# Kernel optimization log

Hardware: AMD Instinct MI355X
Metric: run time of the kernel (lower is better)

## Reference

```python
import jax, jax.numpy as jnp
import numpy as np
from jax import lax

B, E, H, L, P, IMG, NCLS = 8, 768, 12, 12, 16, 224, 1000
D = E // H
MLP = 4 * E
SCALE = D ** -0.5
NPATCH = (IMG // P) ** 2  # 196
N = NPATCH + 1             # 197 with cls token
INIT_VAL = 0.1


def _ln(x, g, b, eps=1e-5):
    mu = jnp.mean(x, -1, keepdims=True)
    var = jnp.mean((x - mu) ** 2, -1, keepdims=True)
    return (x - mu) / jnp.sqrt(var + eps) * g + b


def _wasserstein(q, cov_q, k, cov_k):
    # 2-Wasserstein distance matrix between diagonal Gaussians (STOSA style)
    mean_term = (-2.0 * jnp.einsum('bhnd,bhmd->bhnm', q, k)
                 + jnp.sum(q * q, -1)[..., :, None]
                 + jnp.sum(k * k, -1)[..., None, :])
    sq_q = jnp.sqrt(jnp.clip(cov_q, 1e-24))
    sq_k = jnp.sqrt(jnp.clip(cov_k, 1e-24))
    cov_term = (-2.0 * jnp.einsum('bhnd,bhmd->bhnm', sq_q, sq_k)
                + jnp.sum(cov_q, -1)[..., :, None]
                + jnp.sum(cov_k, -1)[..., None, :])
    return mean_term + cov_term


def _patch_embed(x, w, b):
    # x: [B,3,IMG,IMG], w: [E,3,P,P] -> [B, NPATCH, E]
    y = lax.conv_general_dilated(x, w, (P, P), 'VALID',
                                 dimension_numbers=('NCHW', 'OIHW', 'NCHW'))
    y = y + b[None, :, None, None]
    return y.reshape(x.shape[0], E, -1).transpose(0, 2, 1)


def _mlp(x, w1, b1, w2, b2):
    return jax.nn.gelu(x @ w1.T + b1, approximate=False) @ w2.T + b2


def setup_inputs() -> dict:
    key = jax.random.key(0)
    ks = jax.random.split(key, 32)
    s = 0.02
    inp = {
        'x': jax.random.normal(ks[0], (B, 3, IMG, IMG), jnp.float32),
        'rel_pos_bias': jax.random.normal(ks[1], (H, N, N), jnp.float32),
        'patch_w': jax.random.normal(ks[2], (E, 3, P, P), jnp.float32) * s,
        'patch_b': jnp.zeros((E,), jnp.float32),
        'cov_patch_w': jax.random.normal(ks[3], (E, 3, P, P), jnp.float32) * s,
        'cov_patch_b': jnp.zeros((E,), jnp.float32),
        'cls_tok': jax.random.normal(ks[4], (1, 1, E), jnp.float32) * s,
        'cov_cls_tok': jax.random.normal(ks[5], (1, 1, E), jnp.float32) * s,
        'norm1_g': jnp.ones((L, E), jnp.float32),
        'norm1_b': jnp.zeros((L, E), jnp.float32),
        'qkv_w': jax.random.normal(ks[6], (L, 3 * E, E), jnp.float32) * s,
        'q_bias': jnp.zeros((L, E), jnp.float32),
        'v_bias': jnp.zeros((L, E), jnp.float32),
        'cov_q_bias': jnp.zeros((L, E), jnp.float32),
        'cov_v_bias': jnp.zeros((L, E), jnp.float32),
        'proj_w': jax.random.normal(ks[7], (L, E, E), jnp.float32) * s,
        'proj_b': jnp.zeros((L, E), jnp.float32),
        'cov_proj_w': jax.random.normal(ks[8], (L, E, E), jnp.float32) * s,
        'cov_proj_b': jnp.zeros((L, E), jnp.float32),
        'gamma1': jnp.full((L, E), INIT_VAL, jnp.float32),
        'gamma2': jnp.full((L, E), INIT_VAL, jnp.float32),
        'norm2_g': jnp.ones((L, E), jnp.float32),
        'norm2_b': jnp.zeros((L, E), jnp.float32),
        'fc1_w': jax.random.normal(ks[9], (L, MLP, E), jnp.float32) * s,
        'fc1_b': jnp.zeros((L, MLP), jnp.float32),
        'fc2_w': jax.random.normal(ks[10], (L, E, MLP), jnp.float32) * s,
        'fc2_b': jnp.zeros((L, E), jnp.float32),
        'fc_norm_g': jnp.ones((E,), jnp.float32),
        'fc_norm_b': jnp.zeros((E,), jnp.float32),
        'head_w': jax.random.normal(ks[11], (NCLS, E), jnp.float32) * s,
        'head_b': jnp.zeros((NCLS,), jnp.float32),
    }
    # fix_init_weight rescaling: proj / cov_proj / fc2 divided by sqrt(2*layer_id)
    resc = 1.0 / jnp.sqrt(2.0 * jnp.arange(1, L + 1, dtype=jnp.float32))
    inp['proj_w'] = inp['proj_w'] * resc[:, None, None]
    inp['cov_proj_w'] = inp['cov_proj_w'] * resc[:, None, None]
    inp['fc2_w'] = inp['fc2_w'] * resc[:, None, None]
    return inp


def reference(x, rel_pos_bias, patch_w, patch_b, cov_patch_w, cov_patch_b,
              cls_tok, cov_cls_tok, norm1_g, norm1_b, qkv_w, q_bias, v_bias,
              cov_q_bias, cov_v_bias, proj_w, proj_b, cov_proj_w, cov_proj_b,
              gamma1, gamma2, norm2_g, norm2_b, fc1_w, fc1_b, fc2_w, fc2_b,
              fc_norm_g, fc_norm_b, head_w, head_b):
    b = x.shape[0]
    xm = _patch_embed(x, patch_w, patch_b)
    xc = _patch_embed(x, cov_patch_w, cov_patch_b)
    xm = jnp.concatenate([jnp.broadcast_to(cls_tok, (b, 1, E)), xm], 1)
    xc = jnp.concatenate([jnp.broadcast_to(cov_cls_tok, (b, 1, E)), xc], 1)
    n = xm.shape[1]

    for i in range(L):
        xm_n = _ln(xm, norm1_g[i], norm1_b[i])
        xc_n = _ln(xc, norm1_g[i], norm1_b[i])  # shared norm1, as in source
        qkvb = jnp.concatenate([q_bias[i], jnp.zeros_like(v_bias[i]), v_bias[i]])
        cov_qkvb = jnp.concatenate([cov_q_bias[i], jnp.zeros_like(cov_v_bias[i]), cov_v_bias[i]])
        qkv = (xm_n @ qkv_w[i].T + qkvb).reshape(b, n, 3, H, D).transpose(2, 0, 3, 1, 4)
        q, k, v = qkv[0], qkv[1], qkv[2]
        # NOTE: source (bug-faithfully) uses qkv.weight for the cov path too
        cqkv = jax.nn.elu(xc_n @ qkv_w[i].T + cov_qkvb) + 1.0
        cqkv = cqkv.reshape(b, n, 3, H, D).transpose(2, 0, 3, 1, 4)
        cq, ck, cv = cqkv[0], cqkv[1], cqkv[2]
        q = q * SCALE
        attn = jax.nn.sigmoid(-_wasserstein(q, cq, k, ck) + 1e-24)
        attn = jax.nn.softmax(attn + rel_pos_bias, axis=-1)  # [B,H,N,N]
        mean_ctx = jnp.einsum('bhnm,bhmd->bhnd', attn, v).transpose(0, 2, 1, 3).reshape(b, n, E)
        cov_ctx = jnp.einsum('bhnm,bhmd->bhnd', attn * attn, cv).transpose(0, 2, 1, 3).reshape(b, n, E)
        mh = mean_ctx @ proj_w[i].T + proj_b[i]
        ch = cov_ctx @ cov_proj_w[i].T + cov_proj_b[i]
        xm = xm + gamma1[i] * mh
        xm = xm + gamma2[i] * _mlp(_ln(xm, norm2_g[i], norm2_b[i]), fc1_w[i], fc1_b[i], fc2_w[i], fc2_b[i])
        xc = xc + gamma1[i] * ch
        xc = xc + gamma2[i] * _mlp(_ln(xc, norm2_g[i], norm2_b[i]), fc1_w[i], fc1_b[i], fc2_w[i], fc2_b[i])

    t = jnp.mean(xm[:, 1:], axis=1)          # mean pooling over patch tokens
    t = _ln(t, fc_norm_g, fc_norm_b)
    return t @ head_w.T + head_b              # [B, num_classes]
```

## Files before the change

kernel.cpp:

```cpp
#include <hip/hip_runtime.h>
#include <hip/hip_bf16.h>
#include <math.h>

#define BB 8
#define EE 768
#define HH 12
#define LL 12
#define DD 64
#define MLPD 3072
#define NN 197
#define NPATCH 196
#define NCLS 1000
#define NROWS (BB*NN)
#define PROWS (BB*NPATCH)
#define MPAD 1664
#define HTILES 13
#define NBH (BB*HH)
#define NP224 224
#define NP256 256
#define SCALE 0.125f

#define MODE_F32   0
#define MODE_ELU1F 1
#define MODE_GELUB 2
#define MODE_RESF  3

typedef __attribute__((ext_vector_type(8))) short bf16x8;
typedef __attribute__((ext_vector_type(4))) float f32x4;

__device__ __forceinline__ unsigned short f2b(float f) {
    union { __hip_bfloat16 h; unsigned short u; } x;
    x.h = __float2bfloat16(f);
    return x.u;
}

__device__ __forceinline__ float b2f(unsigned short u) {
    union { unsigned int i; float f; } x;
    x.i = ((unsigned int)u) << 16;
    return x.f;
}

#define GLD(gptr, lptr) __builtin_amdgcn_global_load_lds( \
    (const __attribute__((address_space(1))) unsigned int*)(gptr), \
    (__attribute__((address_space(3))) unsigned int*)(lptr), 16, 0, 0)

__global__ __launch_bounds__(256) void mfma_gemm2(
    const unsigned short* __restrict__ A0, const unsigned short* __restrict__ A1,
    const unsigned short* __restrict__ W0, const unsigned short* __restrict__ W1,
    const float* __restrict__ bias0, const float* __restrict__ bias1,
    int K, int Nc, int mode0, int mode1,
    const float* __restrict__ gamma,
    const float* __restrict__ resid0, const float* __restrict__ resid1,
    float* __restrict__ Cf0, float* __restrict__ Cf1,
    unsigned short* __restrict__ Cb0, unsigned short* __restrict__ Cb1)
{
    __shared__ unsigned short lA[128 * 32];
    __shared__ unsigned short lB[128 * 32];
    const int tid  = threadIdx.x;
    const int lane = tid & 63;
    const int wave = tid >> 6;
    const int wm = wave >> 1, wn = wave & 1;
    const int half = blockIdx.y >= HTILES;
    const int mout0 = (blockIdx.y - (half ? HTILES : 0)) * 128;
    const int n0 = blockIdx.x * 128;
    const unsigned short* A = half ? A1 : A0;
    const unsigned short* W = half ? W1 : W0;
    const float* bias = half ? bias1 : bias0;
    const float* resid = half ? resid1 : resid0;
    float* Cf = half ? Cf1 : Cf0;
    unsigned short* Cb = half ? Cb1 : Cb0;
    const int mode = half ? mode1 : mode0;

    const int srow  = lane >> 2;
    const int skoff = (lane & 3) * 8;
    const int fr = lane & 15;
    const int fk = (lane >> 4) * 8;

    f32x4 acc[4][4];
#pragma unroll
    for (int i = 0; i < 4; i++)
#pragma unroll
        for (int j = 0; j < 4; j++) acc[i][j] = (f32x4){0.f, 0.f, 0.f, 0.f};

    for (int k0 = 0; k0 < K; k0 += 32) {
#pragma unroll
        for (int i = 0; i < 2; i++) {
            int chunk = wave * 2 + i;
            int row = chunk * 16 + srow;
            GLD(A + (size_t)(mout0 + row) * K + k0 + skoff, lA + chunk * 512);
            GLD(W + (size_t)(n0 + row) * K + k0 + skoff, lB + chunk * 512);
        }
        __syncthreads();
        bf16x8 a[4], b[4];
#pragma unroll
        for (int t = 0; t < 4; t++) {
            a[t] = *(const bf16x8*)(lA + (wm * 64 + t * 16 + fr) * 32 + fk);
            b[t] = *(const bf16x8*)(lB + (wn * 64 + t * 16 + fr) * 32 + fk);
        }
#pragma unroll
        for (int i = 0; i < 4; i++)
#pragma unroll
            for (int j = 0; j < 4; j++)
                acc[i][j] = __builtin_amdgcn_mfma_f32_16x16x32_bf16(a[i], b[j], acc[i][j], 0, 0, 0);
        __syncthreads();
    }

    const int crow0 = mout0 + wm * 64;
    const int ccol0 = n0 + wn * 64;
    const int lr = (lane >> 4) * 4;
    const int lc = lane & 15;
#pragma unroll
    for (int i = 0; i < 4; i++) {
#pragma unroll
        for (int j = 0; j < 4; j++) {
            int col = ccol0 + j * 16 + lc;
            float bv = bias ? bias[col] : 0.f;
#pragma unroll
            for (int r = 0; r < 4; r++) {
                int row = crow0 + i * 16 + lr + r;
                float v = acc[i][j][r] + bv;
                size_t o = (size_t)row * Nc + col;
                if (mode == MODE_ELU1F) {
                    Cf[o] = (v > 0.f) ? (v + 1.f) : expf(v);
                } else if (mode == MODE_GELUB) {
                    v = 0.5f * v * (1.f + erff(v * 0.70710678118654752f));
                    Cb[o] = f2b(v);
                } else if (mode == MODE_RESF) {
                    Cf[o] = resid[o] + gamma[col] * v;
                } else {
                    Cf[o] = v;
                }
            }
        }
    }
}

__global__ __launch_bounds__(256) void mfma_gemm2_sk(
    const unsigned short* __restrict__ A0, const unsigned short* __restrict__ A1,
    const unsigned short* __restrict__ W0, const unsigned short* __restrict__ W1,
    int K, int Kc, int Nc, int S,
    float* __restrict__ P)
{
    __shared__ unsigned short lA[128 * 32];
    __shared__ unsigned short lB[128 * 32];
    const int tid  = threadIdx.x;
    const int lane = tid & 63;
    const int wave = tid >> 6;
    const int wm = wave >> 1, wn = wave & 1;
    const int half = blockIdx.y >= HTILES;
    const int mout0 = (blockIdx.y - (half ? HTILES : 0)) * 128;
    const int n0 = blockIdx.x * 128;
    const int z = blockIdx.z;
    const int kb = z * Kc;
    const unsigned short* A = half ? A1 : A0;
    const unsigned short* W = half ? W1 : W0;

    const int srow  = lane >> 2;
    const int skoff = (lane & 3) * 8;
    const int fr = lane & 15;
    const int fk = (lane >> 4) * 8;

    f32x4 acc[4][4];
#pragma unroll
    for (int i = 0; i < 4; i++)
#pragma unroll
        for (int j = 0; j < 4; j++) acc[i][j] = (f32x4){0.f, 0.f, 0.f, 0.f};

    for (int k0 = kb; k0 < kb + Kc; k0 += 32) {
#pragma unroll
        for (int i = 0; i < 2; i++) {
            int chunk = wave * 2 + i;
            int row = chunk * 16 + srow;
            GLD(A + (size_t)(mout0 + row) * K + k0 + skoff, lA + chunk * 512);
            GLD(W + (size_t)(n0 + row) * K + k0 + skoff, lB + chunk * 512);
        }
        __syncthreads();
        bf16x8 a[4], b[4];
#pragma unroll
        for (int t = 0; t < 4; t++) {
            a[t] = *(const bf16x8*)(lA + (wm * 64 + t * 16 + fr) * 32 + fk);
            b[t] = *(const bf16x8*)(lB + (wn * 64 + t * 16 + fr) * 32 + fk);
        }
#pragma unroll
        for (int i = 0; i < 4; i++)
#pragma unroll
            for (int j = 0; j < 4; j++)
                acc[i][j] = __builtin_amdgcn_mfma_f32_16x16x32_bf16(a[i], b[j], acc[i][j], 0, 0, 0);
        __syncthreads();
    }

    float* Pout = P + (size_t)(half * S + z) * MPAD * Nc;
    const int crow0 = mout0 + wm * 64;
    const int ccol0 = n0 + wn * 64;
    const int lr = (lane >> 4) * 4;
    const int lc = lane & 15;
#pragma unroll
    for (int i = 0; i < 4; i++) {
#pragma unroll
        for (int j = 0; j < 4; j++) {
            int col = ccol0 + j * 16 + lc;
#pragma unroll
            for (int r = 0; r < 4; r++) {
                int row = crow0 + i * 16 + lr + r;
                Pout[(size_t)row * Nc + col] = acc[i][j][r];
            }
        }
    }
}

__global__ __launch_bounds__(256) void sk_reduce_kernel(
    const float* __restrict__ P, int S, int Nc, int mode,
    const float* __restrict__ bias0, const float* __restrict__ bias1,
    const float* __restrict__ gamma,
    const float* __restrict__ resid0, const float* __restrict__ resid1,
    float* __restrict__ C0, float* __restrict__ C1)
{
    const size_t per = (size_t)MPAD * Nc;
    size_t gi = ((size_t)blockIdx.x * 256 + threadIdx.x) * 4;
    if (gi >= per) return;
    const int half = blockIdx.y;
    const float* p = P + (size_t)half * S * per + gi;
    float4 s = *(const float4*)p;
    for (int z = 1; z < S; z++) {
        float4 q = *(const float4*)(p + (size_t)z * per);
        s.x += q.x; s.y += q.y; s.z += q.z; s.w += q.w;
    }
    const int col = (int)(gi % (size_t)Nc);
    const float* bias = half ? bias1 : bias0;
    float4 bv = *(const float4*)(bias + col);
    s.x += bv.x; s.y += bv.y; s.z += bv.z; s.w += bv.w;
    float* C = half ? C1 : C0;
    if (mode == MODE_RESF) {
        const float* resid = half ? resid1 : resid0;
        float4 rv = *(const float4*)(resid + gi);
        float4 gv = *(const float4*)(gamma + col);
        s.x = rv.x + gv.x * s.x;
        s.y = rv.y + gv.y * s.y;
        s.z = rv.z + gv.z * s.z;
        s.w = rv.w + gv.w * s.w;
    }
    *(float4*)(C + gi) = s;
}

__global__ __launch_bounds__(256) void pre_kernel(
    const float* __restrict__ qkv, const float* __restrict__ cqkv,
    unsigned short* __restrict__ Aq, unsigned short* __restrict__ Bk,
    float* __restrict__ rsum, float* __restrict__ csum,
    unsigned short* __restrict__ vT, unsigned short* __restrict__ cvT)
{
    const int t = blockIdx.x;
    const int bh = blockIdx.y;
    const int b = bh / HH, h = bh % HH;
    const int n0 = t * 64;
    const int lane = threadIdx.x & 63;
    const int w = threadIdx.x >> 6;
    __shared__ unsigned short vs[64][66];
    __shared__ unsigned short cvs[64][66];

    for (int p = 0; p < 16; p++) {
        int nl = p * 4 + w;
        int n = n0 + nl;
        int d = lane;
        size_t arow = ((size_t)bh * NP256 + n) * 128;
        if (n < NN) {
            size_t basei = (size_t)(b * NN + n) * 3 * EE + h * DD + d;
            float q  = qkv[basei];
            float k  = qkv[basei + EE];
            float v  = qkv[basei + 2 * EE];
            float cq = cqkv[basei];
            float ck = cqkv[basei + EE];
            float cv = cqkv[basei + 2 * EE];
            float qs = q * SCALE;
            float sqq = sqrtf(fmaxf(cq, 1e-24f));
            float sqk = sqrtf(fmaxf(ck, 1e-24f));
            Aq[arow + d]      = f2b(qs);
            Aq[arow + 64 + d] = f2b(sqq);
            Bk[arow + d]      = f2b(k);
            Bk[arow + 64 + d] = f2b(sqk);
            vs[nl][d]  = f2b(v);
            cvs[nl][d] = f2b(cv);
            float r = qs * qs + cq;
            float c = k * k + ck;
            for (int off2 = 32; off2 > 0; off2 >>= 1) {
                r += __shfl_down(r, off2);
                c += __shfl_down(c, off2);
            }
            if (d == 0) { rsum[bh * NP256 + n] = r; csum[bh * NP256 + n] = c; }
        } else {
            ((unsigned int*)(Aq + arow))[d] = 0u;
            ((unsigned int*)(Bk + arow))[d] = 0u;
            vs[nl][d] = 0; cvs[nl][d] = 0;
            if (d == 0) { rsum[bh * NP256 + n] = 0.f; csum[bh * NP256 + n] = 0.f; }
        }
    }
    __syncthreads();
    for (int p = 0; p < 16; p++) {
        int dr = p * 4 + w;
        int n = n0 + lane;
        if (n < NP224) {
            vT [((size_t)bh * 64 + dr) * NP224 + n] = vs[lane][dr];
            cvT[((size_t)bh * 64 + dr) * NP224 + n] = cvs[lane][dr];
        }
    }
}

#define PADW 232
__global__ __launch_bounds__(256) void attn_fused(
    const unsigned short* __restrict__ Aq, const unsigned short* __restrict__ Bk,
    const float* __restrict__ rsum, const float* __restrict__ csum,
    const float* __restrict__ rpb,
    const unsigned short* __restrict__ vT, const unsigned short* __restrict__ cvT,
    unsigned short* __restrict__ ctxm, unsigned short* __restrict__ ctxc)
{
    __shared__ unsigned short lA[64 * 32];
    __shared__ unsigned short lB[256 * 32];
    __shared__ unsigned short lB2[128 * 32];
    __shared__ unsigned short pL[64 * PADW];
    const int tid = threadIdx.x, lane = tid & 63, w = tid >> 6;
    const int bh = blockIdx.y;
    const int b = bh / HH, h = bh % HH;
    const int q0 = blockIdx.x * 64;
    const int srow = lane >> 2, skoff = (lane & 3) * 8;
    const int fr = lane & 15, fk = (lane >> 4) * 8;
    const int lr4 = (lane >> 4) * 4;
    const unsigned short* A = Aq + (size_t)bh * NP256 * 128;
    const unsigned short* B = Bk + (size_t)bh * NP256 * 128;

    f32x4 accS[16];
#pragma unroll
    for (int j = 0; j < 16; j++) accS[j] = (f32x4){0.f, 0.f, 0.f, 0.f};

    for (int k0 = 0; k0 < 128; k0 += 32) {
        GLD(A + (size_t)(q0 + w * 16 + srow) * 128 + k0 + skoff, lA + w * 512);
#pragma unroll
        for (int i = 0; i < 4; i++) {
            int chunk = w * 4 + i;
            GLD(B + (size_t)(chunk * 16 + srow) * 128 + k0 + skoff, lB + chunk * 512);
        }
        __syncthreads();
        bf16x8 a = *(const bf16x8*)(lA + (w * 16 + fr) * 32 + fk);
#pragma unroll
        for (int j = 0; j < 16; j++) {
            bf16x8 bb = *(const bf16x8*)(lB + (j * 16 + fr) * 32 + fk);
            accS[j] = __builtin_amdgcn_mfma_f32_16x16x32_bf16(a, bb, accS[j], 0, 0, 0);
        }
        __syncthreads();
    }

    float rs[4];
#pragma unroll
    for (int r = 0; r < 4; r++) rs[r] = rsum[bh * NP256 + q0 + w * 16 + lr4 + r];
    float cs[16];
#pragma unroll
    for (int j = 0; j < 16; j++) cs[j] = csum[bh * NP256 + j * 16 + fr];

#pragma unroll
    for (int r = 0; r < 4; r++) {
        int rowg = q0 + w * 16 + lr4 + r;
        float v[16];
#pragma unroll
        for (int j = 0; j < 16; j++) {
            int col = j * 16 + fr;
            float z = 2.f * accS[j][r] - rs[r] - cs[j] + 1e-24f;
            float s = 1.f / (1.f + expf(-z));
            float rp = (col < NN && rowg < NN) ? rpb[((size_t)h * NN + rowg) * NN + col] : 0.f;
            v[j] = (col < NN) ? (s + rp) : -1e30f;
        }
        float mx = -1e30f;
#pragma unroll
        for (int j = 0; j < 16; j++) mx = fmaxf(mx, v[j]);
        mx = fmaxf(mx, __shfl_xor(mx, 1));
        mx = fmaxf(mx, __shfl_xor(mx, 2));
        mx = fmaxf(mx, __shfl_xor(mx, 4));
        mx = fmaxf(mx, __shfl_xor(mx, 8));
        float sum = 0.f;
#pragma unroll
        for (int j = 0; j < 16; j++) { v[j] = expf(v[j] - mx); sum += v[j]; }
        sum += __shfl_xor(sum, 1);
        sum += __shfl_xor(sum, 2);
        sum += __shfl_xor(sum, 4);
        sum += __shfl_xor(sum, 8);
        float inv = 1.f / sum;
        int rowl = w * 16 + lr4 + r;
#pragma unroll
        for (int j = 0; j < 14; j++)
            pL[rowl * PADW + j * 16 + fr] = f2b(v[j] * inv);
    }

    f32x4 acc2[2][4];
#pragma unroll
    for (int p = 0; p < 2; p++)
#pragma unroll
        for (int j = 0; j < 4; j++) acc2[p][j] = (f32x4){0.f, 0.f, 0.f, 0.f};

    for (int k0 = 0; k0 < NP224; k0 += 32) {
#pragma unroll
        for (int i = 0; i < 2; i++) {
            int chunk = w * 2 + i;
            const unsigned short* src = (chunk < 4)
                ? (vT  + ((size_t)bh * 64 + chunk * 16 + srow) * NP224)
                : (cvT + ((size_t)bh * 64 + (chunk - 4) * 16 + srow) * NP224);
            GLD(src + k0 + skoff, lB2 + chunk * 512);
        }
        __syncthreads();
        bf16x8 ap = *(const bf16x8*)(pL + (w * 16 + fr) * PADW + k0 + fk);
        bf16x8 ap2;
#pragma unroll
        for (int e = 0; e < 8; e++) {
            float pv = b2f((unsigned short)ap[e]);
            ap2[e] = (short)f2b(pv * pv);
        }
#pragma unroll
        for (int j = 0; j < 4; j++) {
            bf16x8 bv = *(const bf16x8*)(lB2 + (j * 16 + fr) * 32 + fk);
            bf16x8 bc = *(const bf16x8*)(lB2 + ((64 + j * 16) + fr) * 32 + fk);
            acc2[0][j] = __builtin_amdgcn_mfma_f32_16x16x32_bf16(ap,  bv, acc2[0][j], 0, 0, 0);
            acc2[1][j] = __builtin_amdgcn_mfma_f32_16x16x32_bf16(ap2, bc, acc2[1][j], 0, 0, 0);
        }
        __syncthreads();
    }

#pragma unroll
    for (int j = 0; j < 4; j++) {
        int d = j * 16 + fr;
#pragma unroll
        for (int r = 0; r < 4; r++) {
            int n = q0 + w * 16 + lr4 + r;
            if (n >= NN) continue;
            size_t o = ((size_t)(b * NN + n)) * EE + h * DD + d;
            ctxm[o] = f2b(acc2[0][j][r]);
            ctxc[o] = f2b(acc2[1][j][r]);
        }
    }
}

__global__ __launch_bounds__(256) void head_kernel(
    const float* __restrict__ pooled, const float* __restrict__ W,
    const float* __restrict__ bias, float* __restrict__ out)
{
    const int wv = threadIdx.x >> 6, lane = threadIdx.x & 63;
    const int c = blockIdx.x * 4 + wv;
    const int b = blockIdx.y;
    if (c >= NCLS) return;
    const float* wr = W + (size_t)c * EE;
    const float* pr = pooled + (size_t)b * EE;
    float s = 0.f;
#pragma unroll
    for (int i = 0; i < 12; i++) s += pr[lane + i * 64] * wr[lane + i * 64];
    for (int off = 32; off > 0; off >>= 1) s += __shfl_down(s, off);
    if (lane == 0) out[(size_t)b * NCLS + c] = s + bias[c];
}

__global__ __launch_bounds__(256) void cvt_kernel(
    const float* __restrict__ src, unsigned short* __restrict__ dst, int n)
{
    int i = (blockIdx.x * 256 + threadIdx.x) * 4;
    if (i >= n) return;
    float4 f = *(const float4*)(src + i);
    ushort4 u;
    u.x = f2b(f.x); u.y = f2b(f.y); u.z = f2b(f.z); u.w = f2b(f.w);
    *(ushort4*)(dst + i) = u;
}

#define W_QKV   0
#define W_PROJ  1769472
#define W_CPROJ 2359296
#define W_FC1   2949120
#define W_FC2   5308416
#define W_TOTAL 7667712

__global__ __launch_bounds__(256) void cvt_layer_kernel(
    const float* __restrict__ qkvw, const float* __restrict__ pw,
    const float* __restrict__ cpw, const float* __restrict__ f1,
    const float* __restrict__ f2, unsigned short* __restrict__ dst)
{
    int i = (blockIdx.x * 256 + threadIdx.x) * 4;
    if (i >= W_TOTAL) return;
    const float* s; int off;
    if (i < W_PROJ)        { s = qkvw; off = W_QKV; }
    else if (i < W_CPROJ)  { s = pw;   off = W_PROJ; }
    else if (i < W_FC1)    { s = cpw;  off = W_CPROJ; }
    else if (i < W_FC2)    { s = f1;   off = W_FC1; }
    else                   { s = f2;   off = W_FC2; }
    float4 f = *(const float4*)(s + (i - off));
    ushort4 u;
    u.x = f2b(f.x); u.y = f2b(f.y); u.z = f2b(f.z); u.w = f2b(f.w);
    *(ushort4*)(dst + i) = u;
}

__global__ __launch_bounds__(256) void im2col_kernel(
    const float* __restrict__ x, unsigned short* __restrict__ col)
{
    int idx = blockIdx.x * 256 + threadIdx.x;
    if (idx >= PROWS * EE) return;
    int c = idx % EE;
    int r = idx / EE;
    int b = r / NPATCH;
    int p = r % NPATCH;
    int ph = p / 14, pw = p % 14;
    int ch = c >> 8;
    int rem = c & 255;
    int i = rem >> 4, j = rem & 15;
    col[idx] = f2b(x[(((size_t)b * 3 + ch) * 224 + (ph * 16 + i)) * 224 + (pw * 16 + j)]);
}

__global__ __launch_bounds__(256) void assemble_kernel(
    const float* __restrict__ tm, const float* __restrict__ tc,
    const float* __restrict__ cls, const float* __restrict__ ccls,
    float* __restrict__ xm, float* __restrict__ xc)
{
    int idx = blockIdx.x * 256 + threadIdx.x;
    if (idx >= NROWS * EE) return;
    int e = idx % EE;
    int r = idx / EE;
    int b = r / NN, n = r % NN;
    if (n == 0) {
        xm[idx] = cls[e];
        xc[idx] = ccls[e];
    } else {
        size_t s = ((size_t)(b * NPATCH + n - 1)) * EE + e;
        xm[idx] = tm[s];
        xc[idx] = tc[s];
    }
}

__global__ __launch_bounds__(256) void ln2_kernel(
    const float* __restrict__ xm, const float* __restrict__ xc,
    unsigned short* __restrict__ y, const float* __restrict__ g,
    const float* __restrict__ bb)
{
    int row = blockIdx.x;
    int tid = threadIdx.x;
    const float* src;
    size_t orow;
    if (row < NROWS) { src = xm + (size_t)row * EE; orow = row; }
    else { src = xc + (size_t)(row - NROWS) * EE; orow = (size_t)(row - NROWS) + MPAD; }
    __shared__ float red[256];
    float v0 = src[tid], v1 = src[tid + 256], v2 = src[tid + 512];
    red[tid] = v0 + v1 + v2;
    __syncthreads();
    for (int s = 128; s > 0; s >>= 1) { if (tid < s) red[tid] += red[tid + s]; __syncthreads(); }
    float mu = red[0] * (1.f / 768.f);
    __syncthreads();
    float d0 = v0 - mu, d1 = v1 - mu, d2 = v2 - mu;
    red[tid] = d0 * d0 + d1 * d1 + d2 * d2;
    __syncthreads();
    for (int s = 128; s > 0; s >>= 1) { if (tid < s) red[tid] += red[tid + s]; __syncthreads(); }
    float rstd = rsqrtf(red[0] * (1.f / 768.f) + 1e-5f);
    unsigned short* yr = y + orow * EE;
    yr[tid]       = f2b(d0 * rstd * g[tid]       + bb[tid]);
    yr[tid + 256] = f2b(d1 * rstd * g[tid + 256] + bb[tid + 256]);
    yr[tid + 512] = f2b(d2 * rstd * g[tid + 512] + bb[tid + 512]);
}

__global__ __launch_bounds__(256) void qkvbias_kernel(
    const float* __restrict__ qb, const float* __restrict__ vb,
    const float* __restrict__ cqb, const float* __restrict__ cvb,
    float* __restrict__ bm, float* __restrict__ bc)
{
    int j = blockIdx.x * 256 + threadIdx.x;
    if (j >= 3 * EE) return;
    float m, c;
    if (j < EE)        { m = qb[j];        c = cqb[j]; }
    else if (j < 2*EE) { m = 0.f;          c = 0.f; }
    else               { m = vb[j - 2*EE]; c = cvb[j - 2*EE]; }
    bm[j] = m;
    bc[j] = c;
}

__global__ __launch_bounds__(256) void pool_ln_kernel(
    const float* __restrict__ xm, float* __restrict__ out,
    const float* __restrict__ g, const float* __restrict__ bb)
{
    int b = blockIdx.x;
    int tid = threadIdx.x;
    __shared__ float red[256];
    float p[3];
#pragma unroll
    for (int i = 0; i < 3; i++) {
        int e = tid + i * 256;
        float s = 0.f;
        for (int n = 1; n < NN; n++) s += xm[((size_t)(b * NN + n)) * EE + e];
        p[i] = s * (1.f / 196.f);
    }
    red[tid] = p[0] + p[1] + p[2];
    __syncthreads();
    for (int s = 128; s > 0; s >>= 1) { if (tid < s) red[tid] += red[tid + s]; __syncthreads(); }
    float mu = red[0] * (1.f / 768.f);
    __syncthreads();
    float d0 = p[0] - mu, d1 = p[1] - mu, d2 = p[2] - mu;
    red[tid] = d0 * d0 + d1 * d1 + d2 * d2;
    __syncthreads();
    for (int s = 128; s > 0; s >>= 1) { if (tid < s) red[tid] += red[tid + s]; __syncthreads(); }
    float rstd = rsqrtf(red[0] * (1.f / 768.f) + 1e-5f);
    out[(size_t)b * EE + tid]       = d0 * rstd * g[tid]       + bb[tid];
    out[(size_t)b * EE + tid + 256] = d1 * rstd * g[tid + 256] + bb[tid + 256];
    out[(size_t)b * EE + tid + 512] = d2 * rstd * g[tid + 512] + bb[tid + 512];
}

extern "C" void kernel_launch(void* const* d_in, const int* in_sizes, int n_in,
                              void* d_out, int out_size, void* d_ws, size_t ws_size,
                              hipStream_t stream)
{
    const float* x        = (const float*)d_in[0];
    const float* rpb      = (const float*)d_in[1];
    const float* patch_w  = (const float*)d_in[2];
    const float* patch_b  = (const float*)d_in[3];
    const float* cpatch_w = (const float*)d_in[4];
    const float* cpatch_b = (const float*)d_in[5];
    const float* cls_tok  = (const float*)d_in[6];
    const float* ccls_tok = (const float*)d_in[7];
    const float* norm1_g  = (const float*)d_in[8];
    const float* norm1_b  = (const float*)d_in[9];
    const float* qkv_w    = (const float*)d_in[10];
    const float* q_bias   = (const float*)d_in[11];
    const float* v_bias   = (const float*)d_in[12];
    const float* cq_bias  = (const float*)d_in[13];
    const float* cv_bias  = (const float*)d_in[14];
    const float* proj_w   = (const float*)d_in[15];
    const float* proj_b   = (const float*)d_in[16];
    const float* cproj_w  = (const float*)d_in[17];
    const float* cproj_b  = (const float*)d_in[18];
    const float* gamma1   = (const float*)d_in[19];
    const float* gamma2   = (const float*)d_in[20];
    const float* norm2_g  = (const float*)d_in[21];
    const float* norm2_b  = (const float*)d_in[22];
    const float* fc1_w    = (const float*)d_in[23];
    const float* fc1_b    = (const float*)d_in[24];
    const float* fc2_w    = (const float*)d_in[25];
    const float* fc2_b    = (const float*)d_in[26];
    const float* fcn_g    = (const float*)d_in[27];
    const float* fcn_b    = (const float*)d_in[28];
    const float* head_w   = (const float*)d_in[29];
    const float* head_b   = (const float*)d_in[30];
    float* out = (float*)d_out;

    char* base = (char*)d_ws;
    size_t off = 0;
    auto alloc = [&](size_t bytes) {
        void* p = base + off;
        off = (off + bytes + 255) & ~(size_t)255;
        return p;
    };
    unsigned short* wbuf  = (unsigned short*)alloc((size_t)W_TOTAL * 2);
    unsigned short* pw_m  = (unsigned short*)alloc((size_t)589824 * 2);
    unsigned short* pw_c  = (unsigned short*)alloc((size_t)589824 * 2);
    float* xm   = (float*)alloc((size_t)MPAD * EE * 4);
    float* xc   = (float*)alloc((size_t)MPAD * EE * 4);
    unsigned short* xn2 = (unsigned short*)alloc((size_t)2 * MPAD * EE * 2);
    float* qkv  = (float*)alloc((size_t)MPAD * 3 * EE * 4);
    float* cqkv = (float*)alloc((size_t)MPAD * 3 * EE * 4);
    unsigned short* hbuf = (unsigned short*)alloc((size_t)2 * MPAD * MLPD * 2);
    unsigned short* Aq  = (unsigned short*)alloc((size_t)NBH * NP256 * 128 * 2);
    unsigned short* Bk  = (unsigned short*)alloc((size_t)NBH * NP256 * 128 * 2);
    unsigned short* vT  = (unsigned short*)alloc((size_t)NBH * 64 * NP224 * 2);
    unsigned short* cvT = (unsigned short*)alloc((size_t)NBH * 64 * NP224 * 2);
    float* rsum = (float*)alloc((size_t)NBH * NP256 * 4);
    float* csum = (float*)alloc((size_t)NBH * NP256 * 4);
    unsigned short* ctx2 = (unsigned short*)alloc((size_t)2 * MPAD * EE * 2);
    unsigned short* colb = (unsigned short*)alloc((size_t)MPAD * EE * 2);
    float* biasq  = (float*)alloc(3 * EE * 4);
    float* biasc  = (float*)alloc(3 * EE * 4);
    float* pooled = (float*)alloc((size_t)BB * EE * 4);
    float* pbuf = (float*)alloc((size_t)2 * 4 * MPAD * EE * 4);
    float* tm = qkv;
    float* tc = cqkv;
    unsigned short* ctxm = ctx2;
    unsigned short* ctxc = ctx2 + (size_t)MPAD * EE;

    dim3 t256(256);
    dim3 gridRed(MPAD * EE / 1024, 2);

    cvt_kernel<<<dim3(589824 / 4 / 256), t256, 0, stream>>>(patch_w, pw_m, 589824);
    cvt_kernel<<<dim3(589824 / 4 / 256), t256, 0, stream>>>(cpatch_w, pw_c, 589824);
    im2col_kernel<<<dim3((PROWS * EE + 255) / 256), t256, 0, stream>>>(x, colb);
    mfma_gemm2_sk<<<dim3(EE / 128, 2 * HTILES, 3), t256, 0, stream>>>(
        colb, colb, pw_m, pw_c, EE, 256, EE, 3, pbuf);
    sk_reduce_kernel<<<gridRed, t256, 0, stream>>>(
        pbuf, 3, EE, MODE_F32, patch_b, cpatch_b, nullptr, nullptr, nullptr, tm, tc);
    assemble_kernel<<<dim3((NROWS * EE + 255) / 256), t256, 0, stream>>>(
        tm, tc, cls_tok, ccls_tok, xm, xc);

    dim3 gridQKV(3 * EE / 128, 2 * HTILES);
    dim3 gridMLP(MLPD / 128, 2 * HTILES);
    dim3 gridPre(4, NBH);
    dim3 gridAttn(4, NBH);
    dim3 gridCvtL((W_TOTAL / 4 + 255) / 256);
    dim3 gridLN(2 * NROWS);
    const unsigned short* xn2c = xn2 + (size_t)MPAD * EE;
    const unsigned short* hbufc = hbuf + (size_t)MPAD * MLPD;

    for (int l = 0; l < LL; l++) {
        cvt_layer_kernel<<<gridCvtL, t256, 0, stream>>>(
            qkv_w + (size_t)l * 3 * EE * EE, proj_w + (size_t)l * EE * EE,
            cproj_w + (size_t)l * EE * EE, fc1_w + (size_t)l * MLPD * EE,
            fc2_w + (size_t)l * EE * MLPD, wbuf);
        qkvbias_kernel<<<dim3(9), t256, 0, stream>>>(
            q_bias + l * EE, v_bias + l * EE, cq_bias + l * EE, cv_bias + l * EE,
            biasq, biasc);

        ln2_kernel<<<gridLN, t256, 0, stream>>>(xm, xc, xn2, norm1_g + l * EE, norm1_b + l * EE);
        mfma_gemm2<<<gridQKV, t256, 0, stream>>>(
            xn2, xn2c, wbuf + W_QKV, wbuf + W_QKV, biasq, biasc, EE, 3 * EE,
            MODE_F32, MODE_ELU1F, nullptr, nullptr, nullptr, qkv, cqkv, nullptr, nullptr);

        pre_kernel<<<gridPre, t256, 0, stream>>>(qkv, cqkv, Aq, Bk, rsum, csum, vT, cvT);
        attn_fused<<<gridAttn, t256, 0, stream>>>(Aq, Bk, rsum, csum, rpb, vT, cvT, ctxm, ctxc);

        mfma_gemm2_sk<<<dim3(EE / 128, 2 * HTILES, 3), t256, 0, stream>>>(
            ctxm, ctxc, wbuf + W_PROJ, wbuf + W_CPROJ, EE, 256, EE, 3, pbuf);
        sk_reduce_kernel<<<gridRed, t256, 0, stream>>>(
            pbuf, 3, EE, MODE_RESF, proj_b + l * EE, cproj_b + l * EE,
            gamma1 + l * EE, xm, xc, xm, xc);

        ln2_kernel<<<gridLN, t256, 0, stream>>>(xm, xc, xn2, norm2_g + l * EE, norm2_b + l * EE);
        mfma_gemm2<<<gridMLP, t256, 0, stream>>>(
            xn2, xn2c, wbuf + W_FC1, wbuf + W_FC1, fc1_b + l * MLPD, fc1_b + l * MLPD,
            EE, MLPD, MODE_GELUB, MODE_GELUB, nullptr, nullptr, nullptr,
            nullptr, nullptr, hbuf, hbuf + (size_t)MPAD * MLPD);
        mfma_gemm2_sk<<<dim3(EE / 128, 2 * HTILES, 4), t256, 0, stream>>>(
            hbuf, hbufc, wbuf + W_FC2, wbuf + W_FC2, MLPD, 768, EE, 4, pbuf);
        sk_reduce_kernel<<<gridRed, t256, 0, stream>>>(
            pbuf, 4, EE, MODE_RESF, fc2_b + l * EE, fc2_b + l * EE,
            gamma2 + l * EE, xm, xc, xm, xc);
    }

    pool_ln_kernel<<<dim3(BB), t256, 0, stream>>>(xm, pooled, fcn_g, fcn_b);
    head_kernel<<<dim3((NCLS + 3) / 4, BB), t256, 0, stream>>>(pooled, head_w, head_b, out);
}
```

Before: 2.880 ms.

## Double-buffer GEMM LDS, fuse split-K reduce with LayerNorm, hoist weight conversion

Three unrelated changes. The GEMM kernels now double-buffer their LDS tiles so the next K-slice loads while MFMAs run on the current one. The split-K reduce is fused with the residual update and the following LayerNorm, which removes the separate ln2 launches inside the layer loop. Weight and bias conversion for all 12 layers now happens once before the loop instead of per layer, at the cost of a larger bf16 weight buffer and doubled LDS per block, which may reduce occupancy.

```diff
diff --git a/kernel.cpp b/kernel.cpp
--- a/kernel.cpp
+++ b/kernel.cpp
@@ -54,8 +54,8 @@
     float* __restrict__ Cf0, float* __restrict__ Cf1,
     unsigned short* __restrict__ Cb0, unsigned short* __restrict__ Cb1)
 {
-    __shared__ unsigned short lA[128 * 32];
-    __shared__ unsigned short lB[128 * 32];
+    __shared__ unsigned short lA[2][128 * 32];
+    __shared__ unsigned short lB[2][128 * 32];
     const int tid  = threadIdx.x;
     const int lane = tid & 63;
     const int wave = tid >> 6;
@@ -76,26 +76,33 @@
     const int fr = lane & 15;
     const int fk = (lane >> 4) * 8;
 
-    f32x4 acc[4][4];
-#pragma unroll
-    for (int i = 0; i < 4; i++)
-#pragma unroll
-        for (int j = 0; j < 4; j++) acc[i][j] = (f32x4){0.f, 0.f, 0.f, 0.f};
-
-    for (int k0 = 0; k0 < K; k0 += 32) {
+    auto stage = [&](int bufi, int k0) {
 #pragma unroll
         for (int i = 0; i < 2; i++) {
             int chunk = wave * 2 + i;
             int row = chunk * 16 + srow;
-            GLD(A + (size_t)(mout0 + row) * K + k0 + skoff, lA + chunk * 512);
-            GLD(W + (size_t)(n0 + row) * K + k0 + skoff, lB + chunk * 512);
-        }
-        __syncthreads();
+            GLD(A + (size_t)(mout0 + row) * K + k0 + skoff, &lA[bufi][chunk * 512]);
+            GLD(W + (size_t)(n0 + row) * K + k0 + skoff, &lB[bufi][chunk * 512]);
+        }
+    };
+
+    f32x4 acc[4][4];
+#pragma unroll
+    for (int i = 0; i < 4; i++)
+#pragma unroll
+        for (int j = 0; j < 4; j++) acc[i][j] = (f32x4){0.f, 0.f, 0.f, 0.f};
+
+    const int NT = K >> 5;
+    stage(0, 0);
+    __syncthreads();
+    int cur = 0;
+    for (int t = 0; t < NT; t++) {
+        if (t + 1 < NT) stage(cur ^ 1, (t + 1) * 32);
         bf16x8 a[4], b[4];
 #pragma unroll
-        for (int t = 0; t < 4; t++) {
-            a[t] = *(const bf16x8*)(lA + (wm * 64 + t * 16 + fr) * 32 + fk);
-            b[t] = *(const bf16x8*)(lB + (wn * 64 + t * 16 + fr) * 32 + fk);
+        for (int q = 0; q < 4; q++) {
+            a[q] = *(const bf16x8*)(&lA[cur][(wm * 64 + q * 16 + fr) * 32 + fk]);
+            b[q] = *(const bf16x8*)(&lB[cur][(wn * 64 + q * 16 + fr) * 32 + fk]);
         }
 #pragma unroll
         for (int i = 0; i < 4; i++)
@@ -103,6 +110,7 @@
             for (int j = 0; j < 4; j++)
                 acc[i][j] = __builtin_amdgcn_mfma_f32_16x16x32_bf16(a[i], b[j], acc[i][j], 0, 0, 0);
         __syncthreads();
+        cur ^= 1;
     }
 
     const int crow0 = mout0 + wm * 64;
@@ -141,8 +149,8 @@
     int K, int Kc, int Nc, int S,
     float* __restrict__ P)
 {
-    __shared__ unsigned short lA[128 * 32];
-    __shared__ unsigned short lB[128 * 32];
+    __shared__ unsigned short lA[2][128 * 32];
+    __shared__ unsigned short lB[2][128 * 32];
     const int tid  = threadIdx.x;
     const int lane = tid & 63;
     const int wave = tid >> 6;
@@ -160,26 +168,33 @@
     const int fr = lane & 15;
     const int fk = (lane >> 4) * 8;
 
-    f32x4 acc[4][4];
-#pragma unroll
-    for (int i = 0; i < 4; i++)
-#pragma unroll
-        for (int j = 0; j < 4; j++) acc[i][j] = (f32x4){0.f, 0.f, 0.f, 0.f};
-
-    for (int k0 = kb; k0 < kb + Kc; k0 += 32) {
+    auto stage = [&](int bufi, int k0) {
 #pragma unroll
         for (int i = 0; i < 2; i++) {
             int chunk = wave * 2 + i;
             int row = chunk * 16 + srow;
-            GLD(A + (size_t)(mout0 + row) * K + k0 + skoff, lA + chunk * 512);
-            GLD(W + (size_t)(n0 + row) * K + k0 + skoff, lB + chunk * 512);
-        }
-        __syncthreads();
+            GLD(A + (size_t)(mout0 + row) * K + k0 + skoff, &lA[bufi][chunk * 512]);
+            GLD(W + (size_t)(n0 + row) * K + k0 + skoff, &lB[bufi][chunk * 512]);
+        }
+    };
+
+    f32x4 acc[4][4];
+#pragma unroll
+    for (int i = 0; i < 4; i++)
+#pragma unroll
+        for (int j = 0; j < 4; j++) acc[i][j] = (f32x4){0.f, 0.f, 0.f, 0.f};
+
+    const int NT = Kc >> 5;
+    stage(0, kb);
+    __syncthreads();
+    int cur = 0;
+    for (int t = 0; t < NT; t++) {
+        if (t + 1 < NT) stage(cur ^ 1, kb + (t + 1) * 32);
         bf16x8 a[4], b[4];
 #pragma unroll
-        for (int t = 0; t < 4; t++) {
-            a[t] = *(const bf16x8*)(lA + (wm * 64 + t * 16 + fr) * 32 + fk);
-            b[t] = *(const bf16x8*)(lB + (wn * 64 + t * 16 + fr) * 32 + fk);
+        for (int q = 0; q < 4; q++) {
+            a[q] = *(const bf16x8*)(&lA[cur][(wm * 64 + q * 16 + fr) * 32 + fk]);
+            b[q] = *(const bf16x8*)(&lB[cur][(wn * 64 + q * 16 + fr) * 32 + fk]);
         }
 #pragma unroll
         for (int i = 0; i < 4; i++)
@@ -187,6 +202,7 @@
             for (int j = 0; j < 4; j++)
                 acc[i][j] = __builtin_amdgcn_mfma_f32_16x16x32_bf16(a[i], b[j], acc[i][j], 0, 0, 0);
         __syncthreads();
+        cur ^= 1;
     }
 
     float* Pout = P + (size_t)(half * S + z) * MPAD * Nc;
@@ -209,10 +225,8 @@
 }
 
 __global__ __launch_bounds__(256) void sk_reduce_kernel(
-    const float* __restrict__ P, int S, int Nc, int mode,
+    const float* __restrict__ P, int S, int Nc,
     const float* __restrict__ bias0, const float* __restrict__ bias1,
-    const float* __restrict__ gamma,
-    const float* __restrict__ resid0, const float* __restrict__ resid1,
     float* __restrict__ C0, float* __restrict__ C1)
 {
     const size_t per = (size_t)MPAD * Nc;
@@ -230,16 +244,51 @@
     float4 bv = *(const float4*)(bias + col);
     s.x += bv.x; s.y += bv.y; s.z += bv.z; s.w += bv.w;
     float* C = half ? C1 : C0;
-    if (mode == MODE_RESF) {
-        const float* resid = half ? resid1 : resid0;
-        float4 rv = *(const float4*)(resid + gi);
-        float4 gv = *(const float4*)(gamma + col);
-        s.x = rv.x + gv.x * s.x;
-        s.y = rv.y + gv.y * s.y;
-        s.z = rv.z + gv.z * s.z;
-        s.w = rv.w + gv.w * s.w;
-    }
     *(float4*)(C + gi) = s;
+}
+
+__global__ __launch_bounds__(256) void sk_reduce_ln(
+    const float* __restrict__ P, int S,
+    const float* __restrict__ bias0, const float* __restrict__ bias1,
+    const float* __restrict__ gamma,
+    const float* __restrict__ resid0, const float* __restrict__ resid1,
+    float* __restrict__ C0, float* __restrict__ C1,
+    const float* __restrict__ lnG, const float* __restrict__ lnB,
+    unsigned short* __restrict__ Y)
+{
+    const int row = blockIdx.x;
+    const int half = blockIdx.y;
+    const int tid = threadIdx.x;
+    const size_t per = (size_t)MPAD * EE;
+    const float* p = P + (size_t)half * S * per + (size_t)row * EE;
+    const float* bias = half ? bias1 : bias0;
+    const float* resid = half ? resid1 : resid0;
+    float* C = half ? C1 : C0;
+    float v[3];
+#pragma unroll
+    for (int i = 0; i < 3; i++) {
+        int e = tid + i * 256;
+        float s = p[e];
+        for (int z = 1; z < S; z++) s += p[(size_t)z * per + e];
+        v[i] = resid[(size_t)row * EE + e] + gamma[e] * (s + bias[e]);
+        C[(size_t)row * EE + e] = v[i];
+    }
+    if (!Y) return;
+    __shared__ float red[256];
+    red[tid] = v[0] + v[1] + v[2];
+    __syncthreads();
+    for (int s2 = 128; s2 > 0; s2 >>= 1) { if (tid < s2) red[tid] += red[tid + s2]; __syncthreads(); }
+    float mu = red[0] * (1.f / 768.f);
+    __syncthreads();
+    float d0 = v[0] - mu, d1 = v[1] - mu, d2 = v[2] - mu;
+    red[tid] = d0 * d0 + d1 * d1 + d2 * d2;
+    __syncthreads();
+    for (int s2 = 128; s2 > 0; s2 >>= 1) { if (tid < s2) red[tid] += red[tid + s2]; __syncthreads(); }
+    float rstd = rsqrtf(red[0] * (1.f / 768.f) + 1e-5f);
+    unsigned short* yr = Y + ((size_t)half * MPAD + row) * EE;
+    yr[tid]       = f2b(d0 * rstd * lnG[tid]       + lnB[tid]);
+    yr[tid + 256] = f2b(d1 * rstd * lnG[tid + 256] + lnB[tid + 256]);
+    yr[tid + 512] = f2b(d2 * rstd * lnG[tid + 512] + lnB[tid + 512]);
 }
 
 __global__ __launch_bounds__(256) void pre_kernel(
@@ -469,23 +518,41 @@
 #define W_FC2   5308416
 #define W_TOTAL 7667712
 
-__global__ __launch_bounds__(256) void cvt_layer_kernel(
+__global__ __launch_bounds__(256) void cvt_all_kernel(
     const float* __restrict__ qkvw, const float* __restrict__ pw,
     const float* __restrict__ cpw, const float* __restrict__ f1,
     const float* __restrict__ f2, unsigned short* __restrict__ dst)
 {
-    int i = (blockIdx.x * 256 + threadIdx.x) * 4;
-    if (i >= W_TOTAL) return;
-    const float* s; int off;
-    if (i < W_PROJ)        { s = qkvw; off = W_QKV; }
-    else if (i < W_CPROJ)  { s = pw;   off = W_PROJ; }
-    else if (i < W_FC1)    { s = cpw;  off = W_CPROJ; }
-    else if (i < W_FC2)    { s = f1;   off = W_FC1; }
-    else                   { s = f2;   off = W_FC2; }
-    float4 f = *(const float4*)(s + (i - off));
+    size_t i = ((size_t)blockIdx.x * 256 + threadIdx.x) * 4;
+    if (i >= (size_t)LL * W_TOTAL) return;
+    int l = (int)(i / W_TOTAL);
+    int r = (int)(i % W_TOTAL);
+    const float* s;
+    if (r < W_PROJ)        s = qkvw + (size_t)l * (3 * EE * EE) + r;
+    else if (r < W_CPROJ)  s = pw   + (size_t)l * (EE * EE)     + (r - W_PROJ);
+    else if (r < W_FC1)    s = cpw  + (size_t)l * (EE * EE)     + (r - W_CPROJ);
+    else if (r < W_FC2)    s = f1   + (size_t)l * (MLPD * EE)   + (r - W_FC1);
+    else                   s = f2   + (size_t)l * (MLPD * EE)   + (r - W_FC2);
+    float4 f = *(const float4*)s;
     ushort4 u;
     u.x = f2b(f.x); u.y = f2b(f.y); u.z = f2b(f.z); u.w = f2b(f.w);
     *(ushort4*)(dst + i) = u;
+}
+
+__global__ __launch_bounds__(256) void qkvbias_all_kernel(
+    const float* __restrict__ qb, const float* __restrict__ vb,
+    const float* __restrict__ cqb, const float* __restrict__ cvb,
+    float* __restrict__ bqc)
+{
+    int l = blockIdx.y;
+    int j = blockIdx.x * 256 + threadIdx.x;
+    if (j >= 3 * EE) return;
+    float m, c;
+    if (j < EE)        { m = qb[l * EE + j];          c = cqb[l * EE + j]; }
+    else if (j < 2*EE) { m = 0.f;                      c = 0.f; }
+    else               { m = vb[l * EE + j - 2 * EE];  c = cvb[l * EE + j - 2 * EE]; }
+    bqc[(size_t)l * 4608 + j]        = m;
+    bqc[(size_t)l * 4608 + 2304 + j] = c;
 }
 
 __global__ __launch_bounds__(256) void im2col_kernel(
@@ -551,21 +618,6 @@
     yr[tid]       = f2b(d0 * rstd * g[tid]       + bb[tid]);
     yr[tid + 256] = f2b(d1 * rstd * g[tid + 256] + bb[tid + 256]);
     yr[tid + 512] = f2b(d2 * rstd * g[tid + 512] + bb[tid + 512]);
-}
-
-__global__ __launch_bounds__(256) void qkvbias_kernel(
-    const float* __restrict__ qb, const float* __restrict__ vb,
-    const float* __restrict__ cqb, const float* __restrict__ cvb,
-    float* __restrict__ bm, float* __restrict__ bc)
-{
-    int j = blockIdx.x * 256 + threadIdx.x;
-    if (j >= 3 * EE) return;
-    float m, c;
-    if (j < EE)        { m = qb[j];        c = cqb[j]; }
-    else if (j < 2*EE) { m = 0.f;          c = 0.f; }
-    else               { m = vb[j - 2*EE]; c = cvb[j - 2*EE]; }
-    bm[j] = m;
-    bc[j] = c;
 }
 
 __global__ __launch_bounds__(256) void pool_ln_kernel(
@@ -642,7 +694,7 @@
         off = (off + bytes + 255) & ~(size_t)255;
         return p;
     };
-    unsigned short* wbuf  = (unsigned short*)alloc((size_t)W_TOTAL * 2);
+    unsigned short* wbuf  = (unsigned short*)alloc((size_t)LL * W_TOTAL * 2);
     unsigned short* pw_m  = (unsigned short*)alloc((size_t)589824 * 2);
     unsigned short* pw_c  = (unsigned short*)alloc((size_t)589824 * 2);
     float* xm   = (float*)alloc((size_t)MPAD * EE * 4);
@@ -659,8 +711,7 @@
     float* csum = (float*)alloc((size_t)NBH * NP256 * 4);
     unsigned short* ctx2 = (unsigned short*)alloc((size_t)2 * MPAD * EE * 2);
     unsigned short* colb = (unsigned short*)alloc((size_t)MPAD * EE * 2);
-    float* biasq  = (float*)alloc(3 * EE * 4);
-    float* biasc  = (float*)alloc(3 * EE * 4);
+    float* bqc    = (float*)alloc((size_t)LL * 2 * 2304 * 4);
     float* pooled = (float*)alloc((size_t)BB * EE * 4);
     float* pbuf = (float*)alloc((size_t)2 * 4 * MPAD * EE * 4);
     float* tm = qkv;
@@ -669,60 +720,71 @@
     unsigned short* ctxc = ctx2 + (size_t)MPAD * EE;
 
     dim3 t256(256);
-    dim3 gridRed(MPAD * EE / 1024, 2);
+    dim3 gridRedE(MPAD * EE / 1024, 2);
+    dim3 gridRedLN(MPAD, 2);
+
+    {
+        size_t tot4 = (size_t)LL * W_TOTAL / 4;
+        cvt_all_kernel<<<dim3((unsigned)((tot4 + 255) / 256)), t256, 0, stream>>>(
+            qkv_w, proj_w, cproj_w, fc1_w, fc2_w, wbuf);
+        qkvbias_all_kernel<<<dim3(9, LL), t256, 0, stream>>>(
+            q_bias, v_bias, cq_bias, cv_bias, bqc);
+    }
 
     cvt_kernel<<<dim3(589824 / 4 / 256), t256, 0, stream>>>(patch_w, pw_m, 589824);
     cvt_kernel<<<dim3(589824 / 4 / 256), t256, 0, stream>>>(cpatch_w, pw_c, 589824);
     im2col_kernel<<<dim3((PROWS * EE + 255) / 256), t256, 0, stream>>>(x, colb);
     mfma_gemm2_sk<<<dim3(EE / 128, 2 * HTILES, 3), t256, 0, stream>>>(
         colb, colb, pw_m, pw_c, EE, 256, EE, 3, pbuf);
-    sk_reduce_kernel<<<gridRed, t256, 0, stream>>>(
-        pbuf, 3, EE, MODE_F32, patch_b, cpatch_b, nullptr, nullptr, nullptr, tm, tc);
+    sk_reduce_kernel<<<gridRedE, t256, 0, stream>>>(
+        pbuf, 3, EE, patch_b, cpatch_b, tm, tc);
     assemble_kernel<<<dim3((NROWS * EE + 255) / 256), t256, 0, stream>>>(
         tm, tc, cls_tok, ccls_tok, xm, xc);
+    ln2_kernel<<<dim3(2 * NROWS), t256, 0, stream>>>(xm, xc, xn2, norm1_g, norm1_b);
 
     dim3 gridQKV(3 * EE / 128, 2 * HTILES);
     dim3 gridMLP(MLPD / 128, 2 * HTILES);
     dim3 gridPre(4, NBH);
     dim3 gridAttn(4, NBH);
-    dim3 gridCvtL((W_TOTAL / 4 + 255) / 256);
-    dim3 gridLN(2 * NROWS);
     const unsigned short* xn2c = xn2 + (size_t)MPAD * EE;
     const unsigned short* hbufc = hbuf + (size_t)MPAD * MLPD;
 
     for (int l = 0; l < LL; l++) {
-        cvt_layer_kernel<<<gridCvtL, t256, 0, stream>>>(
-            qkv_w + (size_t)l * 3 * EE * EE, proj_w + (size_t)l * EE * EE,
-            cproj_w + (size_t)l * EE * EE, fc1_w + (size_t)l * MLPD * EE,
-            fc2_w + (size_t)l * EE * MLPD, wbuf);
-        qkvbias_kernel<<<dim3(9), t256, 0, stream>>>(
-            q_bias + l * EE, v_bias + l * EE, cq_bias + l * EE, cv_bias + l * EE,
-            biasq, biasc);
-
-        ln2_kernel<<<gridLN, t256, 0, stream>>>(xm, xc, xn2, norm1_g + l * EE, norm1_b + l * EE);
+        const unsigned short* wl = wbuf + (size_t)l * W_TOTAL;
+        const float* biasq = bqc + (size_t)l * 4608;
+        const float* biasc = biasq + 2304;
+
         mfma_gemm2<<<gridQKV, t256, 0, stream>>>(
-            xn2, xn2c, wbuf + W_QKV, wbuf + W_QKV, biasq, biasc, EE, 3 * EE,
+            xn2, xn2c, wl + W_QKV, wl + W_QKV, biasq, biasc, EE, 3 * EE,
             MODE_F32, MODE_ELU1F, nullptr, nullptr, nullptr, qkv, cqkv, nullptr, nullptr);
 
         pre_kernel<<<gridPre, t256, 0, stream>>>(qkv, cqkv, Aq, Bk, rsum, csum, vT, cvT);
         attn_fused<<<gridAttn, t256, 0, stream>>>(Aq, Bk, rsum, csum, rpb, vT, cvT, ctxm, ctxc);
 
         mfma_gemm2_sk<<<dim3(EE / 128, 2 * HTILES, 3), t256, 0, stream>>>(
-            ctxm, ctxc, wbuf + W_PROJ, wbuf + W_CPROJ, EE, 256, EE, 3, pbuf);
-        sk_reduce_kernel<<<gridRed, t256, 0, stream>>>(
-            pbuf, 3, EE, MODE_RESF, proj_b + l * EE, cproj_b + l * EE,
-            gamma1 + l * EE, xm, xc, xm, xc);
-
-        ln2_kernel<<<gridLN, t256, 0, stream>>>(xm, xc, xn2, norm2_g + l * EE, norm2_b + l * EE);
+            ctxm, ctxc, wl + W_PROJ, wl + W_CPROJ, EE, 256, EE, 3, pbuf);
+        sk_reduce_ln<<<gridRedLN, t256, 0, stream>>>(
+            pbuf, 3, proj_b + l * EE, cproj_b + l * EE,
+            gamma1 + l * EE, xm, xc, xm, xc,
+            norm2_g + l * EE, norm2_b + l * EE, xn2);
+
         mfma_gemm2<<<gridMLP, t256, 0, stream>>>(
-            xn2, xn2c, wbuf + W_FC1, wbuf + W_FC1, fc1_b + l * MLPD, fc1_b + l * MLPD,
+            xn2, xn2c, wl + W_FC1, wl + W_FC1, fc1_b + l * MLPD, fc1_b + l * MLPD,
             EE, MLPD, MODE_GELUB, MODE_GELUB, nullptr, nullptr, nullptr,
             nullptr, nullptr, hbuf, hbuf + (size_t)MPAD * MLPD);
         mfma_gemm2_sk<<<dim3(EE / 128, 2 * HTILES, 4), t256, 0, stream>>>(
-            hbuf, hbufc, wbuf + W_FC2, wbuf + W_FC2, MLPD, 768, EE, 4, pbuf);
-        sk_reduce_kernel<<<gridRed, t256, 0, stream>>>(
-            pbuf, 4, EE, MODE_RESF, fc2_b + l * EE, fc2_b + l * EE,
-            gamma2 + l * EE, xm, xc, xm, xc);
+            hbuf, hbufc, wl + W_FC2, wl + W_FC2, MLPD, 768, EE, 4, pbuf);
+        if (l + 1 < LL) {
+            sk_reduce_ln<<<gridRedLN, t256, 0, stream>>>(
+                pbuf, 4, fc2_b + l * EE, fc2_b + l * EE,
+                gamma2 + l * EE, xm, xc, xm, xc,
+                norm1_g + (l + 1) * EE, norm1_b + (l + 1) * EE, xn2);
+        } else {
+            sk_reduce_ln<<<gridRedLN, t256, 0, stream>>>(
+                pbuf, 4, fc2_b + l * EE, fc2_b + l * EE,
+                gamma2 + l * EE, xm, xc, xm, xc,
+                nullptr, nullptr, nullptr);
+        }
     }
 
     pool_ln_kernel<<<dim3(BB), t256, 0, stream>>>(xm, pooled, fcn_g, fcn_b);
```

Result: faster. 2.654 ms (-7.9%).
